# Kernel tuning notes

Measured on AMD Instinct MI355X. Metric: run time of the kernel, lower is better.

## Reference

```python
import jax, jax.numpy as jnp
import numpy as np

B, T, D = 4, 4096, 1024

def setup_inputs() -> dict:
    key = jax.random.key(0)
    ks = jax.random.split(key, 8)
    s = 1.0 / np.sqrt(D)
    return {
        "x": jax.random.normal(ks[0], (B, T, D), dtype=jnp.float32),
        # diagonal SSM params (per-channel)
        "A": jax.random.uniform(ks[1], (D,), dtype=jnp.float32, minval=0.5, maxval=0.99),  # stable decay
        "Bp": jax.random.normal(ks[2], (D,), dtype=jnp.float32) * 0.1,
        "Cp": jax.random.normal(ks[3], (D,), dtype=jnp.float32),
        # gate Linear
        "gate_w": jax.random.uniform(ks[4], (D, D), dtype=jnp.float32, minval=-s, maxval=s),
        "gate_b": jnp.zeros((D,), dtype=jnp.float32),
        # out Linear
        "out_w": jax.random.uniform(ks[5], (D, D), dtype=jnp.float32, minval=-s, maxval=s),
        "out_b": jnp.zeros((D,), dtype=jnp.float32),
    }

def _ssm(x, A, Bp, Cp):
    # diagonal linear recurrence: h_t = A*h_{t-1} + Bp*x_t ; y_t = Cp*h_t
    bx = x * Bp  # (B,T,D)
    def step(h, bx_t):
        h = A * h + bx_t  # (B,D)
        return h, h
    h0 = jnp.zeros((x.shape[0], x.shape[2]), dtype=x.dtype)
    _, hs = jax.lax.scan(step, h0, jnp.swapaxes(bx, 0, 1))  # (T,B,D)
    return jnp.swapaxes(hs, 0, 1) * Cp  # (B,T,D)

def reference(x, A, Bp, Cp, gate_w, gate_b, out_w, out_b):
    ssm_out = _ssm(x, A, Bp, Cp)
    gate = jax.nn.sigmoid(jnp.einsum('btd,ed->bte', x, gate_w) + gate_b)
    y = gate * ssm_out
    return jnp.einsum('btd,ed->bte', y, out_w) + out_b
```

## Files before the change

kernel.cpp:

```cpp
#include <hip/hip_runtime.h>
#include <hip/hip_bf16.h>
#include <cstdio>

typedef __hip_bfloat16 bf16;
typedef __bf16 bf16x8 __attribute__((ext_vector_type(8)));
typedef float f32x4 __attribute__((ext_vector_type(4)));

#define B_DIM 4
#define T_DIM 4096
#define D_DIM 1024
#define NC 64
#define LC 64

#define M_DIM (B_DIM * T_DIM)
#define BM 256
#define BN 256
#define BK 32
#define NT (D_DIM / BK)
#define GM (M_DIM / BM)
#define GN (D_DIM / BN)

__global__ __launch_bounds__(256) void cast_w_kernel(
    const float* __restrict__ gw, const float* __restrict__ ow,
    bf16* __restrict__ gw16, bf16* __restrict__ ow16, int n) {
  int i = blockIdx.x * 256 + threadIdx.x;
  if (i < n) {
    gw16[i] = __float2bfloat16(gw[i]);
    ow16[i] = __float2bfloat16(ow[i]);
  }
}

__global__ __launch_bounds__(256) void ssm_pass1(
    const float* __restrict__ x, const float* __restrict__ A,
    const float* __restrict__ Bp, float* __restrict__ hfin) {
  const int tid  = threadIdx.x;
  const int dblk = blockIdx.x & 3;
  const int c    = (blockIdx.x >> 2) & (NC - 1);
  const int b    = blockIdx.x >> 8;
  const int d    = dblk * 256 + tid;
  const float a = A[d], bp = Bp[d];
  const float* p = x + ((size_t)(b * T_DIM + c * LC) * D_DIM + d);
  float h = 0.f;
#pragma unroll 4
  for (int i = 0; i < LC; ++i)
    h = fmaf(a, h, bp * p[(size_t)i * D_DIM]);
  hfin[(b * NC + c) * D_DIM + d] = h;
}

__global__ __launch_bounds__(256) void ssm_pass2(
    const float* __restrict__ A, const float* __restrict__ hfin,
    float* __restrict__ hin) {
  const int idx = blockIdx.x * 256 + threadIdx.x;
  const int d = idx & (D_DIM - 1);
  const int b = idx >> 10;
  float aL = A[d];
#pragma unroll
  for (int s = 0; s < 6; ++s) aL *= aL;
  float h = 0.f;
  for (int c = 0; c < NC; ++c) {
    const int o = (b * NC + c) * D_DIM + d;
    hin[o] = h;
    h = fmaf(aL, h, hfin[o]);
  }
}

__global__ __launch_bounds__(256) void ssm_pass3(
    const float* __restrict__ x, const float* __restrict__ A,
    const float* __restrict__ Bp, const float* __restrict__ Cp,
    const float* __restrict__ hin, bf16* __restrict__ ssm16,
    bf16* __restrict__ x16) {
  const int tid  = threadIdx.x;
  const int dblk = blockIdx.x & 3;
  const int c    = (blockIdx.x >> 2) & (NC - 1);
  const int b    = blockIdx.x >> 8;
  const int d    = dblk * 256 + tid;
  const float a = A[d], bp = Bp[d], cp = Cp[d];
  float h = hin[(b * NC + c) * D_DIM + d];
  const size_t base = (size_t)(b * T_DIM + c * LC) * D_DIM + d;
#pragma unroll 4
  for (int i = 0; i < LC; ++i) {
    const size_t o = base + (size_t)i * D_DIM;
    const float xv = x[o];
    h = fmaf(a, h, bp * xv);
    ssm16[o] = __float2bfloat16(cp * h);
    x16[o]  = __float2bfloat16(xv);
  }
}

template <bool GATE>
__global__ __launch_bounds__(512) void gemm256(
    const bf16* __restrict__ Xm, const bf16* __restrict__ Wm,
    const float* __restrict__ bias, const bf16* __restrict__ ssm,
    bf16* __restrict__ Ybf, float* __restrict__ Yf) {
  __shared__ __align__(16) short LDS[4][16384];

  const int tid  = threadIdx.x;
  const int lane = tid & 63;
  const int wave = tid >> 6;
  const int wm = wave >> 2;
  const int wn = wave & 3;
  const int l15 = lane & 15;
  const int sA = ((lane >> 4) ^ ((l15 >> 1) & 3)) << 3;

  const int bid = blockIdx.x;
  const int swz = (bid & 7) * (GM * GN / 8) + (bid >> 3);
  const int m0 = (swz >> 2) * BM;
  const int n0 = (swz & 3) * BN;

  const int row0 = tid >> 2;
  const int c0   = (tid & 3) ^ ((row0 >> 1) & 3);
  const size_t offA0 = (size_t)(m0 + row0) * D_DIM + c0 * 8;
  const size_t offB0 = (size_t)(n0 + row0) * D_DIM + c0 * 8;

  auto gll = [](const bf16* g, short* l) {
    __builtin_amdgcn_global_load_lds(
        (const __attribute__((address_space(1))) void*)g,
        (__attribute__((address_space(3))) void*)l, 16, 0, 0);
  };
  auto STAGE = [&](int buf, int kt) {
    const size_t ko = (size_t)kt * BK;
    short* b0 = &LDS[buf][0] + wave * 512;
    gll(Xm + offA0 + ko,               b0);
    gll(Xm + offA0 + 128 * D_DIM + ko, b0 + 4096);
    gll(Wm + offB0 + ko,               b0 + 8192);
    gll(Wm + offB0 + 128 * D_DIM + ko, b0 + 12288);
  };

  f32x4 acc[8][4] = {};

  STAGE(0, 0);
  STAGE(1, 1);
  STAGE(2, 2);
  asm volatile("s_waitcnt vmcnt(8)" ::: "memory");
  __builtin_amdgcn_s_barrier();

#define KTILE_BODY(T_, VMSTR, DO_STAGE, DO_BAR)                             \
  {                                                                         \
    const short* bb = &LDS[(T_) & 3][0];                                    \
    bf16x8 a[8], b[4];                                                      \
                      \
    _Pragma("unroll")                                                       \
    for (int i = 0; i < 4; ++i)                                             \
      a[i] = *(const bf16x8*)(bb + (wm * 128 + i * 16 + l15) * BK + sA);    \
    _Pragma("unroll")                                                       \
    for (int j = 0; j < 4; ++j)                                             \
      b[j] = *(const bf16x8*)(bb + 8192 + (wn * 64 + j * 16 + l15) * BK + sA); \
    _Pragma("unroll")                                                       \
    for (int i = 4; i < 8; ++i)                                             \
      a[i] = *(const bf16x8*)(bb + (wm * 128 + i * 16 + l15) * BK + sA);    \
    if (DO_STAGE) STAGE(((T_) + 3) & 3, (T_) + 3);                          \
          \
          \
    __builtin_amdgcn_s_setprio(1);                                          \
    _Pragma("unroll")                                                       \
    for (int i = 0; i < 4; ++i)                                             \
      _Pragma("unroll")                                                     \
      for (int j = 0; j < 4; ++j)                                           \
        acc[i][j] =                                                         \
            __builtin_amdgcn_mfma_f32_16x16x32_bf16(a[i], b[j], acc[i][j], 0, 0, 0); \
    __builtin_amdgcn_s_setprio(0);                                          \
    if (DO_BAR) {                                                           \
      asm volatile("s_waitcnt " VMSTR ::: "memory");                        \
      __builtin_amdgcn_s_barrier();                                         \
    }                                                                       \
    __builtin_amdgcn_s_setprio(1);                                          \
    _Pragma("unroll")                                                       \
    for (int i = 4; i < 8; ++i)                                             \
      _Pragma("unroll")                                                     \
      for (int j = 0; j < 4; ++j)                                           \
        acc[i][j] =                                                         \
            __builtin_amdgcn_mfma_f32_16x16x32_bf16(a[i], b[j], acc[i][j], 0, 0, 0); \
    __builtin_amdgcn_s_setprio(0);                                          \
  }

  for (int t = 0; t < NT - 3; ++t)
    KTILE_BODY(t, "vmcnt(8)", true, true);
  KTILE_BODY(NT - 3, "vmcnt(4)", false, true);
  KTILE_BODY(NT - 2, "vmcnt(0)", false, true);
  KTILE_BODY(NT - 1, "vmcnt(0)", false, false);
#undef KTILE_BODY

#pragma unroll
  for (int i = 0; i < 8; ++i) {
#pragma unroll
    for (int j = 0; j < 4; ++j) {
      const int col = n0 + wn * 64 + j * 16 + l15;
      const float bv = bias[col];
#pragma unroll
      for (int v = 0; v < 4; ++v) {
        const int row = m0 + wm * 128 + i * 16 + (lane >> 4) * 4 + v;
        const size_t o = (size_t)row * D_DIM + col;
        const float val = acc[i][j][v] + bv;
        if (GATE) {
          const float g = 1.f / (1.f + expf(-val));
          Ybf[o] = __float2bfloat16(g * __bfloat162float(ssm[o]));
        } else {
          Yf[o] = val;
        }
      }
    }
  }
}

extern "C" void kernel_launch(void* const* d_in, const int* in_sizes, int n_in,
                              void* d_out, int out_size, void* d_ws, size_t ws_size,
                              hipStream_t stream) {
  const float* x  = (const float*)d_in[0];
  const float* A  = (const float*)d_in[1];
  const float* Bp = (const float*)d_in[2];
  const float* Cp = (const float*)d_in[3];
  const float* gw = (const float*)d_in[4];
  const float* gb = (const float*)d_in[5];
  const float* ow = (const float*)d_in[6];
  const float* ob = (const float*)d_in[7];
  float* out = (float*)d_out;

  const size_t NEED = 73400320;
  if (ws_size < NEED) {
    fprintf(stderr, "kernel_launch: ws_size %zu < needed %zu\n", ws_size, NEED);
    return;
  }
  char* ws = (char*)d_ws;
  bf16*  x16   = (bf16*)(ws);
  bf16*  ssm16 = (bf16*)(ws + 33554432);
  bf16*  gw16  = (bf16*)(ws + 67108864);
  bf16*  ow16  = (bf16*)(ws + 69206016);
  float* hfin  = (float*)(ws + 71303168);
  float* hin   = (float*)(ws + 72351744);

  cast_w_kernel<<<(D_DIM * D_DIM) / 256, 256, 0, stream>>>(gw, ow, gw16, ow16, D_DIM * D_DIM);
  ssm_pass1<<<B_DIM * NC * (D_DIM / 256), 256, 0, stream>>>(x, A, Bp, hfin);
  ssm_pass2<<<(B_DIM * D_DIM) / 256, 256, 0, stream>>>(A, hfin, hin);
  ssm_pass3<<<B_DIM * NC * (D_DIM / 256), 256, 0, stream>>>(x, A, Bp, Cp, hin, ssm16, x16);

  gemm256<true><<<GM * GN, 512, 0, stream>>>(x16, gw16, gb, ssm16, ssm16, nullptr);
  gemm256<false><<<GM * GN, 512, 0, stream>>>(ssm16, ow16, ob, nullptr, nullptr, out);
}
```

Baseline: 130.0 us.

## Switch GEMM to 32x32x16 MFMA with k-octet-major LDS layout

Replaces the 16x16x32 bf16 MFMA tiling with 32x32x16 MFMA instructions, giving each wave a 4x2 grid of 32x32 accumulators. The global-to-LDS staging now stores each tile as column-octet-major slabs, so fragments are read with simple strided offsets and the XOR swizzle is dropped. The aim is fewer MFMA issues and less LDS traffic per FLOP. The unswizzled layout may bring LDS bank conflicts, and the epilogue writes follow a different row pattern.

```diff
diff --git a/kernel.cpp b/kernel.cpp
--- a/kernel.cpp
+++ b/kernel.cpp
@@ -4,7 +4,7 @@
 
 typedef __hip_bfloat16 bf16;
 typedef __bf16 bf16x8 __attribute__((ext_vector_type(8)));
-typedef float f32x4 __attribute__((ext_vector_type(4)));
+typedef float f32x16 __attribute__((ext_vector_type(16)));
 
 #define B_DIM 4
 #define T_DIM 4096
@@ -99,18 +99,23 @@
   const int wave = tid >> 6;
   const int wm = wave >> 2;
   const int wn = wave & 3;
-  const int l15 = lane & 15;
-  const int sA = ((lane >> 4) ^ ((l15 >> 1) & 3)) << 3;
+  const int fr = lane & 31;
+  const int k8 = lane >> 5;
 
   const int bid = blockIdx.x;
   const int swz = (bid & 7) * (GM * GN / 8) + (bid >> 3);
   const int m0 = (swz >> 2) * BM;
   const int n0 = (swz & 3) * BN;
 
-  const int row0 = tid >> 2;
-  const int c0   = (tid & 3) ^ ((row0 >> 1) & 3);
-  const size_t offA0 = (size_t)(m0 + row0) * D_DIM + c0 * 8;
-  const size_t offB0 = (size_t)(n0 + row0) * D_DIM + c0 * 8;
+  size_t offA[2], offB[2];
+#pragma unroll
+  for (int it = 0; it < 2; ++it) {
+    const int L   = it * 512 + tid;
+    const int row = L & 255;
+    const int oct = L >> 8;
+    offA[it] = (size_t)(m0 + row) * D_DIM + oct * 8;
+    offB[it] = (size_t)(n0 + row) * D_DIM + oct * 8;
+  }
 
   auto gll = [](const bf16* g, short* l) {
     __builtin_amdgcn_global_load_lds(
@@ -120,13 +125,16 @@
   auto STAGE = [&](int buf, int kt) {
     const size_t ko = (size_t)kt * BK;
     short* b0 = &LDS[buf][0] + wave * 512;
-    gll(Xm + offA0 + ko,               b0);
-    gll(Xm + offA0 + 128 * D_DIM + ko, b0 + 4096);
-    gll(Wm + offB0 + ko,               b0 + 8192);
-    gll(Wm + offB0 + 128 * D_DIM + ko, b0 + 12288);
+    gll(Xm + offA[0] + ko, b0);
+    gll(Xm + offA[1] + ko, b0 + 4096);
+    gll(Wm + offB[0] + ko, b0 + 8192);
+    gll(Wm + offB[1] + ko, b0 + 12288);
   };
 
-  f32x4 acc[8][4] = {};
+  f32x16 acc[4][2] = {};
+
+  const int aBase = (k8 * 256 + wm * 128 + fr) * 8;
+  const int bBase = 8192 + (k8 * 256 + wn * 64 + fr) * 8;
 
   STAGE(0, 0);
   STAGE(1, 1);
@@ -137,27 +145,27 @@
 #define KTILE_BODY(T_, VMSTR, DO_STAGE, DO_BAR)                             \
   {                                                                         \
     const short* bb = &LDS[(T_) & 3][0];                                    \
-    bf16x8 a[8], b[4];                                                      \
-                      \
-    _Pragma("unroll")                                                       \
-    for (int i = 0; i < 4; ++i)                                             \
-      a[i] = *(const bf16x8*)(bb + (wm * 128 + i * 16 + l15) * BK + sA);    \
-    _Pragma("unroll")                                                       \
-    for (int j = 0; j < 4; ++j)                                             \
-      b[j] = *(const bf16x8*)(bb + 8192 + (wn * 64 + j * 16 + l15) * BK + sA); \
-    _Pragma("unroll")                                                       \
-    for (int i = 4; i < 8; ++i)                                             \
-      a[i] = *(const bf16x8*)(bb + (wm * 128 + i * 16 + l15) * BK + sA);    \
+    bf16x8 a0[4], b0[2], a1[4], b1[2];                                      \
+    _Pragma("unroll")                                                       \
+    for (int i = 0; i < 4; ++i)                                             \
+      a0[i] = *(const bf16x8*)(bb + aBase + i * 256);                       \
+    _Pragma("unroll")                                                       \
+    for (int j = 0; j < 2; ++j)                                             \
+      b0[j] = *(const bf16x8*)(bb + bBase + j * 256);                       \
+    _Pragma("unroll")                                                       \
+    for (int i = 0; i < 4; ++i)                                             \
+      a1[i] = *(const bf16x8*)(bb + aBase + 4096 + i * 256);                \
+    _Pragma("unroll")                                                       \
+    for (int j = 0; j < 2; ++j)                                             \
+      b1[j] = *(const bf16x8*)(bb + bBase + 4096 + j * 256);                \
     if (DO_STAGE) STAGE(((T_) + 3) & 3, (T_) + 3);                          \
-          \
-          \
     __builtin_amdgcn_s_setprio(1);                                          \
     _Pragma("unroll")                                                       \
     for (int i = 0; i < 4; ++i)                                             \
       _Pragma("unroll")                                                     \
-      for (int j = 0; j < 4; ++j)                                           \
-        acc[i][j] =                                                         \
-            __builtin_amdgcn_mfma_f32_16x16x32_bf16(a[i], b[j], acc[i][j], 0, 0, 0); \
+      for (int j = 0; j < 2; ++j)                                           \
+        acc[i][j] = __builtin_amdgcn_mfma_f32_32x32x16_bf16(                \
+            a0[i], b0[j], acc[i][j], 0, 0, 0);                              \
     __builtin_amdgcn_s_setprio(0);                                          \
     if (DO_BAR) {                                                           \
       asm volatile("s_waitcnt " VMSTR ::: "memory");                        \
@@ -165,11 +173,11 @@
     }                                                                       \
     __builtin_amdgcn_s_setprio(1);                                          \
     _Pragma("unroll")                                                       \
-    for (int i = 4; i < 8; ++i)                                             \
+    for (int i = 0; i < 4; ++i)                                             \
       _Pragma("unroll")                                                     \
-      for (int j = 0; j < 4; ++j)                                           \
-        acc[i][j] =                                                         \
-            __builtin_amdgcn_mfma_f32_16x16x32_bf16(a[i], b[j], acc[i][j], 0, 0, 0); \
+      for (int j = 0; j < 2; ++j)                                           \
+        acc[i][j] = __builtin_amdgcn_mfma_f32_32x32x16_bf16(                \
+            a1[i], b1[j], acc[i][j], 0, 0, 0);                              \
     __builtin_amdgcn_s_setprio(0);                                          \
   }
 
@@ -181,16 +189,16 @@
 #undef KTILE_BODY
 
 #pragma unroll
-  for (int i = 0; i < 8; ++i) {
-#pragma unroll
-    for (int j = 0; j < 4; ++j) {
-      const int col = n0 + wn * 64 + j * 16 + l15;
+  for (int i = 0; i < 4; ++i) {
+#pragma unroll
+    for (int j = 0; j < 2; ++j) {
+      const int col = n0 + wn * 64 + j * 32 + fr;
       const float bv = bias[col];
 #pragma unroll
-      for (int v = 0; v < 4; ++v) {
-        const int row = m0 + wm * 128 + i * 16 + (lane >> 4) * 4 + v;
+      for (int r = 0; r < 16; ++r) {
+        const int row = m0 + wm * 128 + i * 32 + (r & 3) + 8 * (r >> 2) + 4 * k8;
         const size_t o = (size_t)row * D_DIM + col;
-        const float val = acc[i][j][v] + bv;
+        const float val = acc[i][j][r] + bv;
         if (GATE) {
           const float g = 1.f / (1.f + expf(-val));
           Ybf[o] = __float2bfloat16(g * __bfloat162float(ssm[o]));
```

After: 169.6 us. 30.4% more time.
